# Performance work log

Hardware: AMD Instinct MI355X
Metric: run time of the kernel (lower is better)

## Reference

```python
import jax, jax.numpy as jnp
import numpy as np

N = 1_000_000
E = 5_000_000
EL = 2_000_000
D = 16


def setup_inputs() -> dict:
    key = jax.random.key(0)
    ks = jax.random.split(key, 8)
    x = jnp.arange(N, dtype=jnp.int64) if jax.config.jax_enable_x64 else jnp.arange(N, dtype=jnp.int32)
    edge_index = jax.random.randint(ks[0], (2, E), 0, N, dtype=jnp.int32)
    edge_label_index = jax.random.randint(ks[1], (2, EL), 0, N, dtype=jnp.int32)
    embed_table = jax.random.normal(ks[2], (N, D), dtype=jnp.float32)
    s1 = 1.0 / np.sqrt(D)
    W1 = jax.random.uniform(ks[3], (D, 16), jnp.float32, -s1, s1)
    b1 = jnp.zeros((16,), jnp.float32)
    W2 = jax.random.uniform(ks[4], (16, 16), jnp.float32, -s1, s1)
    b2 = jnp.zeros((16,), jnp.float32)
    s2 = 1.0 / np.sqrt(32)
    fc_w = jax.random.uniform(ks[5], (32, 1), jnp.float32, -s2, s2)
    fc_b = jax.random.uniform(ks[6], (1,), jnp.float32, -s2, s2)
    return {"x": x, "edge_index": edge_index, "edge_label_index": edge_label_index,
            "embed_table": embed_table, "W1": W1, "b1": b1, "W2": W2, "b2": b2,
            "fc_w": fc_w, "fc_b": fc_b}


def _gcn_conv(h, W, b, src, dst, num_nodes):
    # GCNConv: h' = D^-1/2 (A + I) D^-1/2 (h W) + b, with self-loops added
    h = h @ W  # [N, F]
    loops = jnp.arange(num_nodes, dtype=src.dtype)
    src_f = jnp.concatenate([src, loops])
    dst_f = jnp.concatenate([dst, loops])
    deg = jax.ops.segment_sum(jnp.ones_like(dst_f, dtype=h.dtype), dst_f,
                              num_segments=num_nodes)
    dinv = jax.lax.rsqrt(jnp.where(deg > 0, deg, 1.0))
    norm = dinv[src_f] * dinv[dst_f]  # [E+N]
    msg = h[src_f] * norm[:, None]
    out = jax.ops.segment_sum(msg, dst_f, num_segments=num_nodes)
    return out + b


def reference(x, edge_index, edge_label_index, embed_table, W1, b1, W2, b2, fc_w, fc_b):
    src, dst = edge_index[0], edge_index[1]
    h = embed_table[x]                      # embedding lookup, [N, D]
    h = jax.nn.relu(_gcn_conv(h, W1, b1, src, dst, N))
    z = _gcn_conv(h, W2, b2, src, dst, N)   # [N, 16]
    pair = jnp.concatenate([z[edge_label_index[0]], z[edge_label_index[1]]], axis=-1)  # [EL, 32]
    return pair @ fc_w + fc_b               # [EL, 1]
```

## Files before the change

### kernel.cpp

```cpp
#include <hip/hip_runtime.h>
#include <hip/hip_bf16.h>


typedef __hip_bfloat16 bf16;

#define BW_SHIFT 11
#define BW (1 << BW_SHIFT)
#define NB_MAX 512
#define CAPB 12032
#define CHUNK 8192

__device__ __forceinline__ float bf2f(unsigned short s) {
  unsigned u = ((unsigned)s) << 16; float f; __builtin_memcpy(&f, &u, 4); return f;
}
__device__ __forceinline__ unsigned short f2bf(float f) {
  bf16 b = __float2bfloat16(f); unsigned short s; __builtin_memcpy(&s, &b, 2); return s;
}
__device__ __forceinline__ float4 add4(float4 a, float4 b) {
  return make_float4(a.x + b.x, a.y + b.y, a.z + b.z, a.w + b.w);
}

__device__ __forceinline__ void load8_bf(const bf16* p, float4& lo, float4& hi) {
  uint4 u = *(const uint4*)p;
  lo = make_float4(bf2f((unsigned short)(u.x & 0xffffu)), bf2f((unsigned short)(u.x >> 16)),
                   bf2f((unsigned short)(u.y & 0xffffu)), bf2f((unsigned short)(u.y >> 16)));
  hi = make_float4(bf2f((unsigned short)(u.z & 0xffffu)), bf2f((unsigned short)(u.z >> 16)),
                   bf2f((unsigned short)(u.w & 0xffffu)), bf2f((unsigned short)(u.w >> 16)));
}
__device__ __forceinline__ void store16_bf(bf16* p, const float* h) {
  unsigned short t[16];
#pragma unroll
  for (int j = 0; j < 16; ++j) t[j] = f2bf(h[j]);
  uint4 r0, r1;
  __builtin_memcpy(&r0, &t[0], 16);
  __builtin_memcpy(&r1, &t[8], 16);
  uint4* q = (uint4*)p;
  q[0] = r0; q[1] = r1;
}


__global__ __launch_bounds__(256) void init_kernel(int* __restrict__ bcur) {
  int t = blockIdx.x * 256 + threadIdx.x;
  if (t < NB_MAX) bcur[t * 16] = t * CAPB;
}

__global__ __launch_bounds__(256) void bin_kernel(
    const int* __restrict__ src, const int* __restrict__ dst,
    int* __restrict__ bcur, unsigned* __restrict__ rec, int E) {
  __shared__ int hist[NB_MAX];
  __shared__ int excl[NB_MAX];
  __shared__ int gdel[NB_MAX];
  __shared__ int cur[NB_MAX];
  __shared__ int s[256];
  __shared__ unsigned stage[CHUNK];
  int t = threadIdx.x;
  hist[t] = 0; hist[t + 256] = 0;
  __syncthreads();
  int cb = blockIdx.x * CHUNK;
  int cend = E - cb; if (cend > CHUNK) cend = CHUNK;
#pragma unroll 4
  for (int k = 0; k < CHUNK / 256; ++k) {
    int i = k * 256 + t;
    if (i < cend) atomicAdd(&hist[dst[cb + i] >> BW_SHIFT], 1);
  }
  __syncthreads();
  int a0 = hist[2 * t], a1 = hist[2 * t + 1];
  s[t] = a0 + a1;
  __syncthreads();
  for (int off = 1; off < 256; off <<= 1) {
    int x = (t >= off) ? s[t - off] : 0;
    __syncthreads();
    s[t] += x;
    __syncthreads();
  }
  int e0 = (t == 0) ? 0 : s[t - 1];
  excl[2 * t] = e0; excl[2 * t + 1] = e0 + a0;
  cur[2 * t] = e0;  cur[2 * t + 1] = e0 + a0;
  if (a0) gdel[2 * t]     = atomicAdd(&bcur[(2 * t) * 16], a0)     - e0;
  if (a1) gdel[2 * t + 1] = atomicAdd(&bcur[(2 * t + 1) * 16], a1) - (e0 + a0);
  __syncthreads();
#pragma unroll 4
  for (int k = 0; k < CHUNK / 256; ++k) {
    int i = k * 256 + t;
    if (i < cend) {
      int d = dst[cb + i];
      int b = d >> BW_SHIFT;
      unsigned r = ((unsigned)(d & (BW - 1)) << 20) | (unsigned)src[cb + i];
      int off = atomicAdd(&cur[b], 1);
      stage[off] = r;
    }
  }
  __syncthreads();
  for (int p = t; p < cend; p += 256) {
    int b = 0;
#pragma unroll
    for (int st = 256; st > 0; st >>= 1)
      if (b + st < NB_MAX && excl[b + st] <= p) b += st;
    rec[gdel[b] + p] = stage[p];
  }
}

__global__ __launch_bounds__(256) void csr_kernel(
    const unsigned* __restrict__ rec, const int* __restrict__ bcur,
    int* __restrict__ ptr, int* __restrict__ pend,
    int* __restrict__ srt, int N) {
  __shared__ int cnt[BW];
  __shared__ int s[256];
  int b = blockIdx.x, t = threadIdx.x;
  int rb0 = b * CAPB;
  int rb1 = bcur[b * 16];
  for (int i = t; i < BW; i += 256) cnt[i] = 0;
  __syncthreads();
  for (int j = rb0 + t; j < rb1; j += 256) atomicAdd(&cnt[rec[j] >> 20], 1);
  __syncthreads();
  int sum = 0;
#pragma unroll
  for (int j = 0; j < 8; ++j) sum += cnt[t * 8 + j];
  s[t] = sum;
  __syncthreads();
  for (int off = 1; off < 256; off <<= 1) {
    int x = (t >= off) ? s[t - off] : 0;
    __syncthreads();
    s[t] += x;
    __syncthreads();
  }
  int run = (t == 0) ? 0 : s[t - 1];
  int nb0 = b << BW_SHIFT;
#pragma unroll
  for (int j = 0; j < 8; ++j) {
    int idx = t * 8 + j;
    int c = cnt[idx];
    cnt[idx] = run;
    int node = nb0 + idx;
    if (node < N) { ptr[node] = rb0 + run; pend[node] = rb0 + run + c; }
    run += c;
  }
  __syncthreads();
  for (int j = rb0 + t; j < rb1; j += 256) {
    unsigned r = rec[j];
    int off = atomicAdd(&cnt[r >> 20], 1);
    srt[rb0 + off] = (int)(r & 0xFFFFFu);
  }
}


__global__ __launch_bounds__(256) void embed_mm_kernel(
    const int* __restrict__ x, const float* __restrict__ embed,
    const float* __restrict__ W, const int* __restrict__ ptr,
    const int* __restrict__ pend, bf16* __restrict__ g, int n) {
  __shared__ float Ws[256];
  Ws[threadIdx.x] = W[threadIdx.x];
  __syncthreads();
  int i = blockIdx.x * 256 + threadIdx.x;
  if (i >= n) return;
  float dv = rsqrtf((float)(pend[i] - ptr[i]) + 1.0f);
  int row = x[i];
  const float4* hp = (const float4*)(embed + (size_t)row * 16);
  float4 ha = hp[0], hb = hp[1], hc = hp[2], hd = hp[3];
  float h[16] = {ha.x,ha.y,ha.z,ha.w, hb.x,hb.y,hb.z,hb.w,
                 hc.x,hc.y,hc.z,hc.w, hd.x,hd.y,hd.z,hd.w};
  float o[16];
#pragma unroll
  for (int j = 0; j < 16; ++j) o[j] = 0.f;
#pragma unroll
  for (int k = 0; k < 16; ++k) {
    float hk = h[k];
#pragma unroll
    for (int j = 0; j < 16; ++j) o[j] = fmaf(hk, Ws[k * 16 + j], o[j]);
  }
#pragma unroll
  for (int j = 0; j < 16; ++j) o[j] *= dv;
  store16_bf(g + (size_t)i * 16, o);
}

__global__ __launch_bounds__(256, 6) void gather_mm_kernel(
    const int* __restrict__ ptr, const int* __restrict__ pend,
    const int* __restrict__ srt, const bf16* __restrict__ g1,
    const float* __restrict__ W, const float* __restrict__ bias,
    const float* __restrict__ fcw, float2* __restrict__ quv, int n) {
  __shared__ float Ws[256];
  __shared__ float bs[16];
  __shared__ float cw[32];
  __shared__ float wu2[16];
  __shared__ float wv2[16];
  Ws[threadIdx.x] = W[threadIdx.x];
  if (threadIdx.x < 16) bs[threadIdx.x] = bias[threadIdx.x];
  if (threadIdx.x < 32) cw[threadIdx.x] = fcw[threadIdx.x];
  __syncthreads();
  if (threadIdx.x < 16) {
    float su = 0.f, sv = 0.f;
#pragma unroll
    for (int o = 0; o < 16; ++o) {
      float wk = Ws[threadIdx.x * 16 + o];
      su = fmaf(wk, cw[o], su);
      sv = fmaf(wk, cw[16 + o], sv);
    }
    wu2[threadIdx.x] = su;
    wv2[threadIdx.x] = sv;
  }
  __syncthreads();
  int t = blockIdx.x * 256 + threadIdx.x;
  int d = t >> 1;
  if (d >= n) return;
  int q = t & 1;
  int p0 = ptr[d], p1 = pend[d];
  float dv = rsqrtf((float)(p1 - p0) + 1.0f);
  const bf16* gq = g1 + q * 8;
  float4 c0l, c0h, c1l, c1h;
  load8_bf(g1 + (size_t)d * 16 + q * 8, c0l, c0h);
  c1l = make_float4(0.f, 0.f, 0.f, 0.f);
  c1h = make_float4(0.f, 0.f, 0.f, 0.f);
  int j = p0;
  for (; j + 4 <= p1; j += 4) {
    int s0 = srt[j], s1 = srt[j + 1], s2 = srt[j + 2], s3 = srt[j + 3];
    float4 r0l, r0h, r1l, r1h, r2l, r2h, r3l, r3h;
    load8_bf(gq + (size_t)s0 * 16, r0l, r0h);
    load8_bf(gq + (size_t)s1 * 16, r1l, r1h);
    load8_bf(gq + (size_t)s2 * 16, r2l, r2h);
    load8_bf(gq + (size_t)s3 * 16, r3l, r3h);
    c0l = add4(c0l, add4(r0l, r2l)); c0h = add4(c0h, add4(r0h, r2h));
    c1l = add4(c1l, add4(r1l, r3l)); c1h = add4(c1h, add4(r1h, r3h));
  }
  for (; j < p1; ++j) {
    float4 rl, rh;
    load8_bf(gq + (size_t)srt[j] * 16, rl, rh);
    c1l = add4(c1l, rl); c1h = add4(c1h, rh);
  }
  float4 al = add4(c0l, c1l), ah = add4(c0h, c1h);
  float4 bl = *(const float4*)&bs[q * 8];
  float4 bh = *(const float4*)&bs[q * 8 + 4];
  float4 hl = make_float4(fmaxf(fmaf(dv, al.x, bl.x), 0.f),
                          fmaxf(fmaf(dv, al.y, bl.y), 0.f),
                          fmaxf(fmaf(dv, al.z, bl.z), 0.f),
                          fmaxf(fmaf(dv, al.w, bl.w), 0.f));
  float4 hh = make_float4(fmaxf(fmaf(dv, ah.x, bh.x), 0.f),
                          fmaxf(fmaf(dv, ah.y, bh.y), 0.f),
                          fmaxf(fmaf(dv, ah.z, bh.z), 0.f),
                          fmaxf(fmaf(dv, ah.w, bh.w), 0.f));
  float4 ul = *(const float4*)&wu2[q * 8];
  float4 uh = *(const float4*)&wu2[q * 8 + 4];
  float4 vl = *(const float4*)&wv2[q * 8];
  float4 vh = *(const float4*)&wv2[q * 8 + 4];
  float pu = fmaf(hl.x, ul.x, fmaf(hl.y, ul.y, fmaf(hl.z, ul.z, hl.w * ul.w)));
  pu = fmaf(hh.x, uh.x, fmaf(hh.y, uh.y, fmaf(hh.z, uh.z, fmaf(hh.w, uh.w, pu))));
  float pv = fmaf(hl.x, vl.x, fmaf(hl.y, vl.y, fmaf(hl.z, vl.z, hl.w * vl.w)));
  pv = fmaf(hh.x, vh.x, fmaf(hh.y, vh.y, fmaf(hh.z, vh.z, fmaf(hh.w, vh.w, pv))));
  pu += __shfl_xor(pu, 1, 2);
  pv += __shfl_xor(pv, 1, 2);
  if (q == 0) quv[d] = make_float2(pu * dv, pv * dv);
}

__global__ __launch_bounds__(256) void gather_fin_scalar_kernel(
    const int* __restrict__ ptr, const int* __restrict__ pend,
    const int* __restrict__ srt, const float2* __restrict__ quv,
    const float* __restrict__ bias, const float* __restrict__ fcw,
    float* __restrict__ u, float* __restrict__ v, int n) {
  __shared__ float cu_s, cv_s;
  if (threadIdx.x == 0) {
    float cu = 0.f, cv = 0.f;
    for (int o = 0; o < 16; ++o) {
      float b = bias[o];
      cu = fmaf(b, fcw[o], cu);
      cv = fmaf(b, fcw[16 + o], cv);
    }
    cu_s = cu; cv_s = cv;
  }
  __syncthreads();
  int d = blockIdx.x * 256 + threadIdx.x;
  if (d >= n) return;
  int p0 = ptr[d], p1 = pend[d];
  float dv = rsqrtf((float)(p1 - p0) + 1.0f);
  float2 q0 = quv[d];
  float au0 = q0.x, av0 = q0.y, au1 = 0.f, av1 = 0.f;
  int j = p0;
  for (; j + 4 <= p1; j += 4) {
    int s0 = srt[j], s1 = srt[j + 1], s2 = srt[j + 2], s3 = srt[j + 3];
    float2 r0 = quv[s0], r1 = quv[s1], r2 = quv[s2], r3 = quv[s3];
    au0 += r0.x + r2.x; av0 += r0.y + r2.y;
    au1 += r1.x + r3.x; av1 += r1.y + r3.y;
  }
  for (; j < p1; ++j) {
    float2 r = quv[srt[j]];
    au1 += r.x; av1 += r.y;
  }
  u[d] = fmaf(dv, au0 + au1, cu_s);
  v[d] = fmaf(dv, av0 + av1, cv_s);
}

__global__ __launch_bounds__(256) void predict_kernel(
    const int* __restrict__ eli, const float* __restrict__ u,
    const float* __restrict__ v, const float* __restrict__ fcb,
    float* __restrict__ out, int EL) {
  int e = blockIdx.x * 256 + threadIdx.x;
  if (e >= EL) return;
  int a = eli[e], b = eli[EL + e];
  out[e] = u[a] + v[b] + fcb[0];
}

static inline int cdiv(long long a, long long b) { return (int)((a + b - 1) / b); }

extern "C" void kernel_launch(void* const* d_in, const int* in_sizes, int n_in,
                              void* d_out, int out_size, void* d_ws, size_t ws_size,
                              hipStream_t stream) {
  const int*   x     = (const int*)d_in[0];
  const int*   ei    = (const int*)d_in[1];
  const int*   eli   = (const int*)d_in[2];
  const float* embed = (const float*)d_in[3];
  const float* W1    = (const float*)d_in[4];
  const float* b1    = (const float*)d_in[5];
  const float* W2    = (const float*)d_in[6];
  const float* b2    = (const float*)d_in[7];
  const float* fcw   = (const float*)d_in[8];
  const float* fcb   = (const float*)d_in[9];
  float* out = (float*)d_out;

  const int N  = in_sizes[0];
  const int E  = in_sizes[1] / 2;
  const int EL = in_sizes[2] / 2;
  const int* src = ei;
  const int* dst = ei + E;

  const int NB = cdiv(N, BW);

  size_t ptrB = ((size_t)N * 4 + 255) & ~(size_t)255;
  size_t srtB = ((size_t)NB * CAPB * 4 + 255) & ~(size_t)255;
  size_t bufAB = ((size_t)N * 16 * sizeof(bf16) + 255) & ~(size_t)255;

  char* w = (char*)d_ws;
  int* ptr  = (int*)w;
  int* pend = (int*)(w + ptrB);
  int* srt  = (int*)(w + 2 * ptrB);
  char* bA = w + 2 * ptrB + srtB;
  char* bB = bA + bufAB;

  int* bcur = (int*)bA;
  bf16* g1 = (bf16*)bA;
  unsigned* rec = (unsigned*)bB;
  float2* quv = (float2*)bB;
  float* u = (float*)bA;
  float* v = u + N;

  const int B = 256;

  init_kernel<<<2, B, 0, stream>>>(bcur);
  bin_kernel<<<cdiv(E, CHUNK), B, 0, stream>>>(src, dst, bcur, rec, E);
  csr_kernel<<<NB, B, 0, stream>>>(rec, bcur, ptr, pend, srt, N);

  embed_mm_kernel<<<cdiv(N, B), B, 0, stream>>>(x, embed, W1, ptr, pend, g1, N);
  gather_mm_kernel<<<cdiv((long long)N * 2, B), B, 0, stream>>>(
      ptr, pend, srt, g1, W2, b1, fcw, quv, N);
  gather_fin_scalar_kernel<<<cdiv(N, B), B, 0, stream>>>(
      ptr, pend, srt, quv, b2, fcw, u, v, N);
  predict_kernel<<<cdiv(EL, B), B, 0, stream>>>(eli, u, v, fcb, out, EL);
}
```

Baseline: 463.2 us.

## Halve bucket width for CSR build and split final gather across thread pairs

Bucket width drops from 2048 to 1024 nodes, so the bin kernel uses 1024 buckets and the CSR kernel launches twice as many smaller blocks with less per-block work and more parallelism. The bin kernel's scan and bucket search are widened to match. The final scalar gather now assigns two threads per node, splitting the neighbor loop by parity and combining with a lane shuffle, which doubles the threads available to hide latency on irregular loads. In exchange there are more global atomics per chunk in the bin kernel, and the per-bucket capacity is tighter, so an unusually dense bucket could overflow.

Measured after the change: 469.3 us. Within noise of the previous version (+1.3%).

```diff
diff --git a/kernel.cpp b/kernel.cpp
--- a/kernel.cpp
+++ b/kernel.cpp
@@ -4,10 +4,10 @@
 
 typedef __hip_bfloat16 bf16;
 
-#define BW_SHIFT 11
+#define BW_SHIFT 10
 #define BW (1 << BW_SHIFT)
-#define NB_MAX 512
-#define CAPB 12032
+#define NB_MAX 1024
+#define CAPB 6400
 #define CHUNK 8192
 
 __device__ __forceinline__ float bf2f(unsigned short s) {
@@ -54,7 +54,8 @@
   __shared__ int s[256];
   __shared__ unsigned stage[CHUNK];
   int t = threadIdx.x;
-  hist[t] = 0; hist[t + 256] = 0;
+#pragma unroll
+  for (int k = 0; k < NB_MAX / 256; ++k) hist[t + k * 256] = 0;
   __syncthreads();
   int cb = blockIdx.x * CHUNK;
   int cend = E - cb; if (cend > CHUNK) cend = CHUNK;
@@ -64,8 +65,8 @@
     if (i < cend) atomicAdd(&hist[dst[cb + i] >> BW_SHIFT], 1);
   }
   __syncthreads();
-  int a0 = hist[2 * t], a1 = hist[2 * t + 1];
-  s[t] = a0 + a1;
+  int a0 = hist[4 * t], a1 = hist[4 * t + 1], a2 = hist[4 * t + 2], a3 = hist[4 * t + 3];
+  s[t] = a0 + a1 + a2 + a3;
   __syncthreads();
   for (int off = 1; off < 256; off <<= 1) {
     int x = (t >= off) ? s[t - off] : 0;
@@ -74,10 +75,13 @@
     __syncthreads();
   }
   int e0 = (t == 0) ? 0 : s[t - 1];
-  excl[2 * t] = e0; excl[2 * t + 1] = e0 + a0;
-  cur[2 * t] = e0;  cur[2 * t + 1] = e0 + a0;
-  if (a0) gdel[2 * t]     = atomicAdd(&bcur[(2 * t) * 16], a0)     - e0;
-  if (a1) gdel[2 * t + 1] = atomicAdd(&bcur[(2 * t + 1) * 16], a1) - (e0 + a0);
+  int e1 = e0 + a0, e2 = e1 + a1, e3 = e2 + a2;
+  excl[4 * t] = e0; excl[4 * t + 1] = e1; excl[4 * t + 2] = e2; excl[4 * t + 3] = e3;
+  cur[4 * t] = e0;  cur[4 * t + 1] = e1;  cur[4 * t + 2] = e2;  cur[4 * t + 3] = e3;
+  if (a0) gdel[4 * t]     = atomicAdd(&bcur[(4 * t) * 16], a0)     - e0;
+  if (a1) gdel[4 * t + 1] = atomicAdd(&bcur[(4 * t + 1) * 16], a1) - e1;
+  if (a2) gdel[4 * t + 2] = atomicAdd(&bcur[(4 * t + 2) * 16], a2) - e2;
+  if (a3) gdel[4 * t + 3] = atomicAdd(&bcur[(4 * t + 3) * 16], a3) - e3;
   __syncthreads();
 #pragma unroll 4
   for (int k = 0; k < CHUNK / 256; ++k) {
@@ -94,7 +98,7 @@
   for (int p = t; p < cend; p += 256) {
     int b = 0;
 #pragma unroll
-    for (int st = 256; st > 0; st >>= 1)
+    for (int st = 512; st > 0; st >>= 1)
       if (b + st < NB_MAX && excl[b + st] <= p) b += st;
     rec[gdel[b] + p] = stage[p];
   }
@@ -109,13 +113,14 @@
   int b = blockIdx.x, t = threadIdx.x;
   int rb0 = b * CAPB;
   int rb1 = bcur[b * 16];
-  for (int i = t; i < BW; i += 256) cnt[i] = 0;
+#pragma unroll
+  for (int k = 0; k < BW / 256; ++k) cnt[t + k * 256] = 0;
   __syncthreads();
   for (int j = rb0 + t; j < rb1; j += 256) atomicAdd(&cnt[rec[j] >> 20], 1);
   __syncthreads();
   int sum = 0;
 #pragma unroll
-  for (int j = 0; j < 8; ++j) sum += cnt[t * 8 + j];
+  for (int j = 0; j < 4; ++j) sum += cnt[t * 4 + j];
   s[t] = sum;
   __syncthreads();
   for (int off = 1; off < 256; off <<= 1) {
@@ -127,8 +132,8 @@
   int run = (t == 0) ? 0 : s[t - 1];
   int nb0 = b << BW_SHIFT;
 #pragma unroll
-  for (int j = 0; j < 8; ++j) {
-    int idx = t * 8 + j;
+  for (int j = 0; j < 4; ++j) {
+    int idx = t * 4 + j;
     int c = cnt[idx];
     cnt[idx] = run;
     int node = nb0 + idx;
@@ -266,25 +271,32 @@
     cu_s = cu; cv_s = cv;
   }
   __syncthreads();
-  int d = blockIdx.x * 256 + threadIdx.x;
+  int t = blockIdx.x * 256 + threadIdx.x;
+  int d = t >> 1;
   if (d >= n) return;
+  int q = t & 1;
   int p0 = ptr[d], p1 = pend[d];
   float dv = rsqrtf((float)(p1 - p0) + 1.0f);
-  float2 q0 = quv[d];
-  float au0 = q0.x, av0 = q0.y, au1 = 0.f, av1 = 0.f;
-  int j = p0;
-  for (; j + 4 <= p1; j += 4) {
-    int s0 = srt[j], s1 = srt[j + 1], s2 = srt[j + 2], s3 = srt[j + 3];
-    float2 r0 = quv[s0], r1 = quv[s1], r2 = quv[s2], r3 = quv[s3];
-    au0 += r0.x + r2.x; av0 += r0.y + r2.y;
-    au1 += r1.x + r3.x; av1 += r1.y + r3.y;
-  }
-  for (; j < p1; ++j) {
+  float au0 = 0.f, av0 = 0.f, au1 = 0.f, av1 = 0.f;
+  if (q == 0) { float2 q0 = quv[d]; au0 = q0.x; av0 = q0.y; }
+  int j = p0 + q;
+  for (; j + 2 < p1; j += 4) {
+    int s0 = srt[j], s1 = srt[j + 2];
+    float2 r0 = quv[s0], r1 = quv[s1];
+    au0 += r0.x; av0 += r0.y;
+    au1 += r1.x; av1 += r1.y;
+  }
+  for (; j < p1; j += 2) {
     float2 r = quv[srt[j]];
-    au1 += r.x; av1 += r.y;
-  }
-  u[d] = fmaf(dv, au0 + au1, cu_s);
-  v[d] = fmaf(dv, av0 + av1, cv_s);
+    au0 += r.x; av0 += r.y;
+  }
+  float au = au0 + au1, av = av0 + av1;
+  au += __shfl_xor(au, 1, 2);
+  av += __shfl_xor(av, 1, 2);
+  if (q == 0) {
+    u[d] = fmaf(dv, au, cu_s);
+    v[d] = fmaf(dv, av, cv_s);
+  }
 }
 
 __global__ __launch_bounds__(256) void predict_kernel(
@@ -342,14 +354,14 @@
 
   const int B = 256;
 
-  init_kernel<<<2, B, 0, stream>>>(bcur);
+  init_kernel<<<4, B, 0, stream>>>(bcur);
   bin_kernel<<<cdiv(E, CHUNK), B, 0, stream>>>(src, dst, bcur, rec, E);
   csr_kernel<<<NB, B, 0, stream>>>(rec, bcur, ptr, pend, srt, N);
 
   embed_mm_kernel<<<cdiv(N, B), B, 0, stream>>>(x, embed, W1, ptr, pend, g1, N);
   gather_mm_kernel<<<cdiv((long long)N * 2, B), B, 0, stream>>>(
       ptr, pend, srt, g1, W2, b1, fcw, quv, N);
-  gather_fin_scalar_kernel<<<cdiv(N, B), B, 0, stream>>>(
+  gather_fin_scalar_kernel<<<cdiv((long long)N * 2, B), B, 0, stream>>>(
       ptr, pend, srt, quv, b2, fcw, u, v, N);
   predict_kernel<<<cdiv(EL, B), B, 0, stream>>>(eli, u, v, fcb, out, EL);
 }
```
